# Kernel tuning notes

Measured on AMD Instinct MI355X. Metric: run time of the kernel, lower is better.

Reference implementation:

```python
import jax, jax.numpy as jnp
import numpy as np

VOCAB, D_MODEL, NHEAD, NLAYER, DIM_FF, MAX_LEN = 32000, 1024, 16, 6, 4096, 1024
B, L = 8, 1024
PAD_ID = 0
EPS = 1e-5


def _ln(x, g, b):
    m = x.mean(-1, keepdims=True)
    v = x.var(-1, keepdims=True)
    return (x - m) / jnp.sqrt(v + EPS) * g + b


def _mha(x, Wqkv, bqkv, Wo, bo, kpm):
    # x: [B,L,D]; Wqkv: [3D,D]; kpm: [B,L] bool (True = padded key)
    Bx, Lx, D = x.shape
    dh = D // NHEAD
    qkv = x @ Wqkv.T + bqkv                       # [B,L,3D]
    q, k, v = jnp.split(qkv, 3, axis=-1)
    sp = lambda t: t.reshape(Bx, Lx, NHEAD, dh).transpose(0, 2, 1, 3)  # [B,H,L,dh]
    q, k, v = sp(q), sp(k), sp(v)
    scores = jnp.einsum('bhqd,bhkd->bhqk', q, k) * (dh ** -0.5)
    scores = jnp.where(kpm[:, None, None, :], jnp.asarray(-1e9, scores.dtype), scores)
    attn = jax.nn.softmax(scores, axis=-1)        # explicit weights, as ForceWeightsMHA demands
    o = jnp.einsum('bhqk,bhkd->bhqd', attn, v)
    o = o.transpose(0, 2, 1, 3).reshape(Bx, Lx, D)
    return o @ Wo.T + bo


def setup_inputs() -> dict:
    key = jax.random.key(0)
    ks = jax.random.split(key, 20)
    s = 0.02
    n = lambda k, shp: (jax.random.normal(k, shp, dtype=jnp.float32) * s)
    inp = {
        'input_ids': jax.random.randint(ks[0], (B, L), 0, VOCAB, dtype=jnp.int64) if jax.config.jax_enable_x64 else jax.random.randint(ks[0], (B, L), 0, VOCAB).astype(jnp.int32),
        'tok_emb': n(ks[1], (VOCAB, D_MODEL)),
        'pos_emb': n(ks[2], (MAX_LEN, D_MODEL)),
        'Wqkv': n(ks[3], (NLAYER, 3 * D_MODEL, D_MODEL)),
        'bqkv': jnp.zeros((NLAYER, 3 * D_MODEL), jnp.float32),
        'Wo': n(ks[4], (NLAYER, D_MODEL, D_MODEL)),
        'bo': jnp.zeros((NLAYER, D_MODEL), jnp.float32),
        'ln1_g': jnp.ones((NLAYER, D_MODEL), jnp.float32),
        'ln1_b': jnp.zeros((NLAYER, D_MODEL), jnp.float32),
        'W1': n(ks[5], (NLAYER, DIM_FF, D_MODEL)),
        'b1': jnp.zeros((NLAYER, DIM_FF), jnp.float32),
        'W2': n(ks[6], (NLAYER, D_MODEL, DIM_FF)),
        'b2': jnp.zeros((NLAYER, D_MODEL), jnp.float32),
        'ln2_g': jnp.ones((NLAYER, D_MODEL), jnp.float32),
        'ln2_b': jnp.zeros((NLAYER, D_MODEL), jnp.float32),
        'head_ln_g': jnp.ones((D_MODEL,), jnp.float32),
        'head_ln_b': jnp.zeros((D_MODEL,), jnp.float32),
        'head_W': n(ks[7], (MAX_LEN, D_MODEL)),
        'head_b': jnp.zeros((MAX_LEN,), jnp.float32),
    }
    return inp


def reference(input_ids, tok_emb, pos_emb, Wqkv, bqkv, Wo, bo, ln1_g, ln1_b,
              W1, b1, W2, b2, ln2_g, ln2_b, head_ln_g, head_ln_b, head_W, head_b):
    Bx, Lx = input_ids.shape
    x = tok_emb[input_ids] + pos_emb[None, :Lx]           # [B,L,D]
    kpm = (input_ids == PAD_ID).at[:, 0].set(False)        # key padding mask, col 0 forced valid
    for i in range(NLAYER):                                # post-norm encoder layer (PyTorch default)
        x = _ln(x + _mha(x, Wqkv[i], bqkv[i], Wo[i], bo[i], kpm), ln1_g[i], ln1_b[i])
        ff = jax.nn.gelu(x @ W1[i].T + b1[i], approximate=False) @ W2[i].T + b2[i]
        x = _ln(x + ff, ln2_g[i], ln2_b[i])
    cls = x[:, 0, :]                                       # [B,D]
    return _ln(cls, head_ln_g, head_ln_b) @ head_W.T + head_b  # [B,MAX_LEN]
```

## Files before the change

### kernel.cpp

```cpp
#include <hip/hip_runtime.h>
#include <cstdint>

#define D_MODEL 1024
#define NHEAD   16
#define NLAYER  6
#define DIM_FF  4096
#define SEQ_B   8
#define SEQ_L   1024
#define TOKENS  (SEQ_B*SEQ_L)

typedef __bf16 v8bf  __attribute__((ext_vector_type(8)));
typedef __bf16 v4bf  __attribute__((ext_vector_type(4)));
typedef float  v4f   __attribute__((ext_vector_type(4)));

__device__ __forceinline__ void gl_lds16(const void* g, void* l) {
  __builtin_amdgcn_global_load_lds(
      (const __attribute__((address_space(1))) void*)g,
      (__attribute__((address_space(3))) void*)l, 16, 0, 0);
}

__global__ __launch_bounds__(256) void f2b_kernel(const float4* __restrict__ in,
                                                  ushort4* __restrict__ out, long n4) {
  long i = (long)blockIdx.x * 256 + threadIdx.x;
  long stride = (long)gridDim.x * 256;
  for (; i < n4; i += stride) {
    float4 v = in[i];
    v4bf r = { (__bf16)v.x, (__bf16)v.y, (__bf16)v.z, (__bf16)v.w };
    out[i] = *(ushort4*)&r;
  }
}

__global__ __launch_bounds__(256) void embed_kernel(const int* __restrict__ ids,
    const float4* __restrict__ tok, const float4* __restrict__ pos,
    float4* __restrict__ X, ushort4* __restrict__ Xb) {
  long i = (long)blockIdx.x * 256 + threadIdx.x;
  int d4 = (int)(i & 255);
  long bl = i >> 8;
  int l = (int)(bl & (SEQ_L - 1));
  int id = ids[bl];
  float4 t = tok[(long)id * 256 + d4];
  float4 p = pos[(long)l * 256 + d4];
  float4 v = {t.x + p.x, t.y + p.y, t.z + p.z, t.w + p.w};
  X[i] = v;
  v4bf r = { (__bf16)v.x, (__bf16)v.y, (__bf16)v.z, (__bf16)v.w };
  Xb[i] = *(ushort4*)&r;
}

__global__ __launch_bounds__(256) void maskb_kernel(const int* __restrict__ ids,
                                                    float* __restrict__ mb) {
  int i = blockIdx.x * 256 + threadIdx.x;
  mb[i] = (ids[i] == 0 && (i & 1023) != 0) ? -1e9f : 0.f;
}

template<int EPI>
__global__ __launch_bounds__(256) void gemm128(
    const unsigned short* __restrict__ A,
    const unsigned short* __restrict__ W,
    const float* __restrict__ bias,
    float* __restrict__ Cf, unsigned short* __restrict__ Cb,
    unsigned short* __restrict__ Vt,
    int M, int N, int K) {
  __shared__ unsigned short As[128 * 32];
  __shared__ unsigned short Bs[128 * 32];
  int tid = threadIdx.x;
  int wave = tid >> 6, lane = tid & 63;
  int l15 = lane & 15, quad = lane >> 4;

  int id = blockIdx.y * gridDim.x + blockIdx.x;
  int xcd = id & 7, sidx = id >> 3;
  int mt = xcd * 8 + (sidx & 7);
  int nt = sidx >> 3;
  int m0 = mt * 128, n0 = nt * 128;
  int wm = (wave >> 1) * 64, wn = (wave & 1) * 64;

  int srow = tid >> 2;
  int ssl  = (tid & 3) ^ ((srow >> 1) & 3);
  int sc8  = ssl << 3;
  const unsigned short* Ag0 = A + (long)(m0 + srow) * K + sc8;
  const unsigned short* Ag1 = A + (long)(m0 + srow + 64) * K + sc8;
  const unsigned short* Wg0 = W + (long)(n0 + srow) * K + sc8;
  const unsigned short* Wg1 = W + (long)(n0 + srow + 64) * K + sc8;
  unsigned short* As0 = As + tid * 8;
  unsigned short* As1 = As + tid * 8 + 2048;
  unsigned short* Bs0 = Bs + tid * 8;
  unsigned short* Bs1 = Bs + tid * 8 + 2048;

  const unsigned short* afp[4];
  const unsigned short* bfp[4];
  #pragma unroll
  for (int i = 0; i < 4; ++i) {
    int r = wm + i * 16 + l15;
    afp[i] = &As[r * 32 + ((quad ^ ((r >> 1) & 3)) << 3)];
    int rb = wn + i * 16 + l15;
    bfp[i] = &Bs[rb * 32 + ((quad ^ ((rb >> 1) & 3)) << 3)];
  }

  v4f acc[4][4];
  #pragma unroll
  for (int i = 0; i < 4; ++i)
    #pragma unroll
    for (int j = 0; j < 4; ++j) acc[i][j] = (v4f){0.f, 0.f, 0.f, 0.f};

  int ksteps = K >> 5;
  for (int ks = 0; ks < ksteps; ++ks) {
    int k0 = ks << 5;
    __syncthreads();
    gl_lds16(Ag0 + k0, As0);
    gl_lds16(Ag1 + k0, As1);
    gl_lds16(Wg0 + k0, Bs0);
    gl_lds16(Wg1 + k0, Bs1);
    __syncthreads();
    v8bf af[4], bf[4];
    #pragma unroll
    for (int i = 0; i < 4; ++i) af[i] = *(const v8bf*)afp[i];
    #pragma unroll
    for (int j = 0; j < 4; ++j) bf[j] = *(const v8bf*)bfp[j];
    #pragma unroll
    for (int i = 0; i < 4; ++i)
      #pragma unroll
      for (int j = 0; j < 4; ++j)
        acc[i][j] = __builtin_amdgcn_mfma_f32_16x16x32_bf16(af[i], bf[j], acc[i][j], 0, 0, 0);
  }

  #pragma unroll
  for (int i = 0; i < 4; ++i) {
    int crow0 = m0 + wm + i * 16 + quad * 4;
    #pragma unroll
    for (int j = 0; j < 4; ++j) {
      int col = n0 + wn + j * 16 + l15;
      float bv = bias[col];
      if (EPI == 3 && col >= 2048) {
        int hc = (col - 2048) >> 6, d = (col - 2048) & 63;
        int bb = crow0 >> 10, l = crow0 & 1023;
        v4bf pk = { (__bf16)(acc[i][j][0] + bv), (__bf16)(acc[i][j][1] + bv),
                    (__bf16)(acc[i][j][2] + bv), (__bf16)(acc[i][j][3] + bv) };
        *(ushort4*)&Vt[((long)((bb * 16 + hc) * 64 + d)) * 1024 + l] = *(ushort4*)&pk;
      } else {
        #pragma unroll
        for (int r = 0; r < 4; ++r) {
          float v = acc[i][j][r] + bv;
          if (EPI == 1) v = 0.5f * v * (1.f + erff(v * 0.70710678118f));
          long idx = (long)(crow0 + r) * N + col;
          if (EPI == 0) Cf[idx] = v;
          else          ((__bf16*)Cb)[idx] = (__bf16)v;
        }
      }
    }
  }
}

#define MM16(AF, BF, FO) \
  { _Pragma("unroll") for (int f_ = 0; f_ < 4; ++f_) { \
      _Pragma("unroll") for (int j_ = 0; j_ < 4; ++j_) \
        acc[(FO)+f_][j_] = __builtin_amdgcn_mfma_f32_16x16x32_bf16(AF[f_], BF[j_], acc[(FO)+f_][j_], 0, 0, 0); } }

#define STA(c,h,kt) { const unsigned short* s_ = pA + (long)(m0 + (h)*128)*K + ((long)(kt)<<6); \
  gl_lds16(s_,                 dAs + (c)*16384 + (h)*8192); \
  gl_lds16(s_ + ((long)K<<6),  dAs + (c)*16384 + (h)*8192 + 4096); }
#define STB(c,h,kt) { const unsigned short* s_ = pW + (long)(n0 + (h)*128)*K + ((long)(kt)<<6); \
  gl_lds16(s_,                 dBs + (c)*16384 + (h)*8192); \
  gl_lds16(s_ + ((long)K<<6),  dBs + (c)*16384 + (h)*8192 + 4096); }

#define LGKM0  asm volatile("s_waitcnt lgkmcnt(0)" ::: "memory")
#define VMCNT4 asm volatile("s_waitcnt vmcnt(4)" ::: "memory")
#define BARR   __builtin_amdgcn_s_barrier()
#define SCHED0 __builtin_amdgcn_sched_barrier(0)

template<int EPI>
__global__ __launch_bounds__(512, 2) void gemm256(
    const unsigned short* __restrict__ A,
    const unsigned short* __restrict__ W,
    const float* __restrict__ bias,
    unsigned short* __restrict__ Cb,
    unsigned short* __restrict__ Vt,
    int M, int N, int K) {
  __shared__ unsigned short As[2][16384];
  __shared__ unsigned short Bs[2][16384];
  int tid = threadIdx.x;
  int wave = tid >> 6, lane = tid & 63;
  int l15 = lane & 15, quad = lane >> 4;
  int wm = wave >> 2;
  int wn = wave & 3;

  int id = blockIdx.y * gridDim.x + blockIdx.x;
  int xcd = id & 7, sidx = id >> 3;
  int mt = xcd * 4 + (sidx & 3);
  int nt = sidx >> 2;
  int m0 = mt * 256, n0 = nt * 256;

  int srow = tid >> 3;
  int scol = ((tid & 7) ^ ((tid >> 4) & 7)) << 3;
  const unsigned short* pA = A + (long)srow * K + scol;
  const unsigned short* pW = W + (long)srow * K + scol;
  unsigned short* dAs = &As[0][0] + (tid << 3);
  unsigned short* dBs = &Bs[0][0] + (tid << 3);

  int offA[8], offB[4];
  #pragma unroll
  for (int f = 0; f < 8; ++f) {
    int r = wm * 128 + f * 16 + l15;
    offA[f] = r * 64 + ((quad ^ ((r >> 1) & 7)) << 3);
  }
  #pragma unroll
  for (int j = 0; j < 4; ++j) {
    int r = wn * 64 + j * 16 + l15;
    offB[j] = r * 64 + ((quad ^ ((r >> 1) & 7)) << 3);
  }

  v4f acc[8][4];
  #pragma unroll
  for (int f = 0; f < 8; ++f)
    #pragma unroll
    for (int j = 0; j < 4; ++j) acc[f][j] = (v4f){0.f, 0.f, 0.f, 0.f};

  int KT = K >> 6;
  STA(0, 0, 0); STA(0, 1, 0); STB(0, 0, 0); STB(0, 1, 0);
  STA(1, 0, 1); STA(1, 1, 1);
  VMCNT4; BARR; SCHED0;

  const unsigned short* as0 = &As[0][0];
  const unsigned short* bs0 = &Bs[0][0];
  const unsigned short* as1 = &As[1][0];
  const unsigned short* bs1 = &Bs[1][0];

  for (int tb = 0; tb < KT; tb += 2) {
    int kt2 = (tb + 2 < KT) ? tb + 2 : KT - 1;
    int kt3 = (tb + 3 < KT) ? tb + 3 : KT - 1;
    v8bf aA[4], aB[4], aC[4], aD[4], bA[4], bB[4];
    #pragma unroll
    for (int f = 0; f < 4; ++f) aA[f] = *(const v8bf*)(as0 + offA[f]);
    #pragma unroll
    for (int j = 0; j < 4; ++j) bA[j] = *(const v8bf*)(bs0 + offB[j]);
    #pragma unroll
    for (int j = 0; j < 4; ++j) bB[j] = *(const v8bf*)(bs0 + (offB[j] ^ 32));
    STB(1, 0, tb + 1);
    __builtin_amdgcn_s_setprio(1); MM16(aA, bA, 0); __builtin_amdgcn_s_setprio(0);
    #pragma unroll
    for (int f = 0; f < 4; ++f) aB[f] = *(const v8bf*)(as0 + (offA[f] ^ 32));
    STB(1, 1, tb + 1);
    __builtin_amdgcn_s_setprio(1); MM16(aB, bB, 0); __builtin_amdgcn_s_setprio(0);
    LGKM0; BARR; SCHED0;
    #pragma unroll
    for (int f = 0; f < 4; ++f) aC[f] = *(const v8bf*)(as0 + offA[4 + f]);
    #pragma unroll
    for (int f = 0; f < 4; ++f) aD[f] = *(const v8bf*)(as0 + (offA[4 + f] ^ 32));
    STB(0, 0, kt2);
    __builtin_amdgcn_s_setprio(1); MM16(aC, bA, 4); __builtin_amdgcn_s_setprio(0);
    STB(0, 1, kt2);
    __builtin_amdgcn_s_setprio(1); MM16(aD, bB, 4); __builtin_amdgcn_s_setprio(0);
    LGKM0; VMCNT4; BARR; SCHED0;
    #pragma unroll
    for (int f = 0; f < 4; ++f) aA[f] = *(const v8bf*)(as1 + offA[f]);
    #pragma unroll
    for (int j = 0; j < 4; ++j) bA[j] = *(const v8bf*)(bs1 + offB[j]);
    #pragma unroll
    for (int j = 0; j < 4; ++j) bB[j] = *(const v8bf*)(bs1 + (offB[j] ^ 32));
    STA(0, 0, kt2);
    __builtin_amdgcn_s_setprio(1); MM16(aA, bA, 0); __builtin_amdgcn_s_setprio(0);
    #pragma unroll
    for (int f = 0; f < 4; ++f) aB[f] = *(const v8bf*)(as1 + (offA[f] ^ 32));
    #pragma unroll
    for (int f = 0; f < 4; ++f) aC[f] = *(const v8bf*)(as1 + offA[4 + f]);
    #pragma unroll
    for (int f = 0; f < 4; ++f) aD[f] = *(const v8bf*)(as1 + (offA[4 + f] ^ 32));
    STA(0, 1, kt2);
    __builtin_amdgcn_s_setprio(1); MM16(aB, bB, 0); __builtin_amdgcn_s_setprio(0);
    LGKM0; BARR; SCHED0;
    STA(1, 0, kt3);
    __builtin_amdgcn_s_setprio(1); MM16(aC, bA, 4); __builtin_amdgcn_s_setprio(0);
    STA(1, 1, kt3);
    __builtin_amdgcn_s_setprio(1); MM16(aD, bB, 4); __builtin_amdgcn_s_setprio(0);
    VMCNT4; BARR; SCHED0;
  }

  #pragma unroll
  for (int f = 0; f < 8; ++f) {
    int crow0 = m0 + wm * 128 + f * 16 + quad * 4;
    #pragma unroll
    for (int j = 0; j < 4; ++j) {
      int col = n0 + wn * 64 + j * 16 + l15;
      float bv = bias[col];
      if (EPI == 3 && col >= 2048) {
        int hc = (col - 2048) >> 6, d = (col - 2048) & 63;
        int bb = crow0 >> 10, l = crow0 & 1023;
        v4bf pk = { (__bf16)(acc[f][j][0] + bv), (__bf16)(acc[f][j][1] + bv),
                    (__bf16)(acc[f][j][2] + bv), (__bf16)(acc[f][j][3] + bv) };
        *(ushort4*)&Vt[((long)((bb * 16 + hc) * 64 + d)) * 1024 + l] = *(ushort4*)&pk;
      } else {
        #pragma unroll
        for (int r = 0; r < 4; ++r) {
          float v = acc[f][j][r] + bv;
          if (EPI == 1) v = 0.5f * v * (1.f + erff(v * 0.70710678118f));
          ((__bf16*)Cb)[(long)(crow0 + r) * N + col] = (__bf16)v;
        }
      }
    }
  }
}

#define PSP 72
__global__ __launch_bounds__(256) void attn2(
    const unsigned short* __restrict__ QKVb,
    const unsigned short* __restrict__ Vtg,
    const float* __restrict__ mb,
    unsigned short* __restrict__ Ob) {
  __shared__ unsigned short Ks[64 * 64];
  __shared__ unsigned short Vs[64 * 64];
  __shared__ unsigned short Ps[4][16 * PSP];
  int tid = threadIdx.x, wave = tid >> 6, lane = tid & 63;
  int l15 = lane & 15, quad = lane >> 4;
  int b = blockIdx.z, h = blockIdx.y, q0 = blockIdx.x * 64;

  int qrow = q0 + wave * 16 + l15;
  const unsigned short* qb = QKVb + (long)(b * 1024 + qrow) * 3072 + h * 64;
  v8bf gq0 = *(const v8bf*)(qb + quad * 8);
  v8bf gq1 = *(const v8bf*)(qb + 32 + quad * 8);

  v8bf bones;
  #pragma unroll
  for (int j = 0; j < 8; ++j) bones[j] = (l15 == 0) ? (__bf16)1.0f : (__bf16)0.0f;

  float m_run[4], l_run[4];
  v4f O[4];
  #pragma unroll
  for (int r = 0; r < 4; ++r) { m_run[r] = -1e30f; l_run[r] = 0.f; }
  #pragma unroll
  for (int j = 0; j < 4; ++j) O[j] = (v4f){0.f, 0.f, 0.f, 0.f};

  const unsigned short* kgb = QKVb + (long)b * 1024 * 3072 + 1024 + h * 64;
  const unsigned short* vgb = Vtg + (long)((b * 16 + h) * 64) * 1024;
  const float* mrow = mb + b * 1024;

  int srow = tid >> 3;
  int ssl  = (tid & 7) ^ (srow & 7);
  int ph0 = (quad ^ (l15 & 7)) << 3;
  int ph1 = ((quad + 4) ^ (l15 & 7)) << 3;
  const float SC = 0.18033688011112042f;

  for (int k0 = 0; k0 < SEQ_L; k0 += 64) {
    __syncthreads();
    gl_lds16(kgb + (long)(k0 + srow) * 3072 + ssl * 8, &Ks[tid * 8]);
    gl_lds16(kgb + (long)(k0 + srow + 32) * 3072 + ssl * 8, &Ks[tid * 8 + 2048]);
    gl_lds16(vgb + (long)srow * 1024 + k0 + ssl * 8, &Vs[tid * 8]);
    gl_lds16(vgb + (long)(srow + 32) * 1024 + k0 + ssl * 8, &Vs[tid * 8 + 2048]);
    __syncthreads();

    float p[4][4], mr[4];
    #pragma unroll
    for (int r = 0; r < 4; ++r) mr[r] = -1e30f;
    #pragma unroll
    for (int t = 0; t < 4; ++t) {
      int kr = t * 16 + l15;
      v8bf kf0 = *(const v8bf*)&Ks[kr * 64 + ph0];
      v8bf kf1 = *(const v8bf*)&Ks[kr * 64 + ph1];
      v4f s = (v4f){0.f, 0.f, 0.f, 0.f};
      s = __builtin_amdgcn_mfma_f32_16x16x32_bf16(gq0, kf0, s, 0, 0, 0);
      s = __builtin_amdgcn_mfma_f32_16x16x32_bf16(gq1, kf1, s, 0, 0, 0);
      float bv = mrow[k0 + kr];
      #pragma unroll
      for (int r = 0; r < 4; ++r) {
        float sv = fmaf(s[r], SC, bv);
        p[t][r] = sv;
        mr[r] = fmaxf(mr[r], sv);
      }
    }
    #pragma unroll
    for (int r = 0; r < 4; ++r) {
      mr[r] = fmaxf(mr[r], __shfl_xor(mr[r], 1, 64));
      mr[r] = fmaxf(mr[r], __shfl_xor(mr[r], 2, 64));
      mr[r] = fmaxf(mr[r], __shfl_xor(mr[r], 4, 64));
      mr[r] = fmaxf(mr[r], __shfl_xor(mr[r], 8, 64));
    }
    float alpha[4];
    #pragma unroll
    for (int r = 0; r < 4; ++r) {
      float mn = fmaxf(m_run[r], mr[r]);
      alpha[r] = __builtin_amdgcn_exp2f(m_run[r] - mn);
      m_run[r] = mn;
    }
    #pragma unroll
    for (int t = 0; t < 4; ++t)
      #pragma unroll
      for (int r = 0; r < 4; ++r)
        p[t][r] = __builtin_amdgcn_exp2f(p[t][r] - m_run[r]);

    #pragma unroll
    for (int t = 0; t < 4; ++t)
      #pragma unroll
      for (int r = 0; r < 4; ++r)
        ((__bf16*)Ps[wave])[(quad * 4 + r) * PSP + t * 16 + l15] = (__bf16)p[t][r];
    v8bf pa0 = *(const v8bf*)&Ps[wave][l15 * PSP + quad * 8];
    v8bf pa1 = *(const v8bf*)&Ps[wave][l15 * PSP + 32 + quad * 8];

    v4f ss = (v4f){0.f, 0.f, 0.f, 0.f};
    ss = __builtin_amdgcn_mfma_f32_16x16x32_bf16(pa0, bones, ss, 0, 0, 0);
    ss = __builtin_amdgcn_mfma_f32_16x16x32_bf16(pa1, bones, ss, 0, 0, 0);

    #pragma unroll
    for (int j = 0; j < 4; ++j)
      #pragma unroll
      for (int r = 0; r < 4; ++r) O[j][r] *= alpha[r];
    #pragma unroll
    for (int j = 0; j < 4; ++j) {
      v8bf vf0 = *(const v8bf*)&Vs[(j * 16 + l15) * 64 + ph0];
      v8bf vf1 = *(const v8bf*)&Vs[(j * 16 + l15) * 64 + ph1];
      O[j] = __builtin_amdgcn_mfma_f32_16x16x32_bf16(pa0, vf0, O[j], 0, 0, 0);
      O[j] = __builtin_amdgcn_mfma_f32_16x16x32_bf16(pa1, vf1, O[j], 0, 0, 0);
    }
    #pragma unroll
    for (int r = 0; r < 4; ++r)
      l_run[r] = l_run[r] * alpha[r] + __shfl(ss[r], quad << 4, 64);
  }

  int qd = q0 + wave * 16 + quad * 4;
  #pragma unroll
  for (int r = 0; r < 4; ++r) {
    float inv = 1.f / l_run[r];
    #pragma unroll
    for (int j = 0; j < 4; ++j)
      ((__bf16*)Ob)[(long)(b * 1024 + qd + r) * 1024 + h * 64 + j * 16 + l15] =
          (__bf16)(O[j][r] * inv);
  }
}

__global__ __launch_bounds__(256) void add_ln(
    const float* __restrict__ Xin, const float* __restrict__ Yin,
    const float* __restrict__ g, const float* __restrict__ bta,
    float* __restrict__ outF, unsigned short* __restrict__ outB,
    long in_stride, long out_stride) {
  int row = blockIdx.x;
  const float* x = Xin + (long)row * in_stride;
  const float* y = Yin ? Yin + (long)row * 1024 : nullptr;
  int tid = threadIdx.x;
  float v[4];
  float s = 0.f, s2 = 0.f;
  #pragma unroll
  for (int j = 0; j < 4; ++j) {
    int d = j * 256 + tid;
    float t = x[d] + (y ? y[d] : 0.f);
    v[j] = t; s += t; s2 += t * t;
  }
  __shared__ float red[8];
  int lane = tid & 63, wave = tid >> 6;
  #pragma unroll
  for (int o = 32; o > 0; o >>= 1) { s += __shfl_down(s, o, 64); s2 += __shfl_down(s2, o, 64); }
  if (lane == 0) { red[wave] = s; red[4 + wave] = s2; }
  __syncthreads();
  s  = red[0] + red[1] + red[2] + red[3];
  s2 = red[4] + red[5] + red[6] + red[7];
  float mean = s * (1.f / 1024.f);
  float var  = s2 * (1.f / 1024.f) - mean * mean;
  float rstd = rsqrtf(var + 1e-5f);
  float* of = outF + (long)row * out_stride;
  unsigned short* ob = outB ? outB + (long)row * out_stride : nullptr;
  #pragma unroll
  for (int j = 0; j < 4; ++j) {
    int d = j * 256 + tid;
    float o = (v[j] - mean) * rstd * g[d] + bta[d];
    of[d] = o;
    if (ob) ((__bf16*)ob)[d] = (__bf16)o;
  }
}

__global__ __launch_bounds__(256) void head_kernel(
    const float* __restrict__ cls, const float* __restrict__ hW,
    const float* __restrict__ hb, float* __restrict__ out) {
  int n = blockIdx.x * 256 + threadIdx.x;
  int b = blockIdx.y;
  const float4* c4 = (const float4*)(cls + b * 1024);
  const float4* w4 = (const float4*)(hW + (long)n * 1024);
  float s = 0.f;
  #pragma unroll 8
  for (int d = 0; d < 256; ++d) {
    float4 a = c4[d], w = w4[d];
    s += a.x * w.x + a.y * w.y + a.z * w.z + a.w * w.w;
  }
  out[b * 1024 + n] = s + hb[n];
}

extern "C" void kernel_launch(void* const* d_in, const int* in_sizes, int n_in,
                              void* d_out, int out_size, void* d_ws, size_t ws_size,
                              hipStream_t stream) {
  const int*   ids  = (const int*)d_in[0];
  const float* tok  = (const float*)d_in[1];
  const float* pos  = (const float*)d_in[2];
  const float* Wqkv = (const float*)d_in[3];
  const float* bqkv = (const float*)d_in[4];
  const float* Wo   = (const float*)d_in[5];
  const float* bo   = (const float*)d_in[6];
  const float* ln1g = (const float*)d_in[7];
  const float* ln1b = (const float*)d_in[8];
  const float* W1   = (const float*)d_in[9];
  const float* b1   = (const float*)d_in[10];
  const float* W2   = (const float*)d_in[11];
  const float* b2   = (const float*)d_in[12];
  const float* ln2g = (const float*)d_in[13];
  const float* ln2b = (const float*)d_in[14];
  const float* hlng = (const float*)d_in[15];
  const float* hlnb = (const float*)d_in[16];
  const float* hW   = (const float*)d_in[17];
  const float* hb   = (const float*)d_in[18];
  float* out = (float*)d_out;

  char* ws = (char*)d_ws;
  size_t off = 0;
  auto alloc = [&](size_t bytes) {
    char* p = ws + off;
    off = (off + bytes + 255) & ~(size_t)255;
    return p;
  };
  unsigned short* Wqkv_b = (unsigned short*)alloc((size_t)NLAYER*3072*1024*2);
  unsigned short* Wo_b   = (unsigned short*)alloc((size_t)NLAYER*1024*1024*2);
  unsigned short* W1_b   = (unsigned short*)alloc((size_t)NLAYER*4096*1024*2);
  unsigned short* W2_b   = (unsigned short*)alloc((size_t)NLAYER*1024*4096*2);
  float*          X      = (float*)alloc((size_t)TOKENS*1024*4);
  unsigned short* Xb     = (unsigned short*)alloc((size_t)TOKENS*1024*2);
  unsigned short* Qb     = (unsigned short*)alloc((size_t)TOKENS*3072*2);
  unsigned short* Vtg    = (unsigned short*)alloc((size_t)TOKENS*1024*2);
  float*          Y      = (float*)alloc((size_t)TOKENS*1024*4);
  unsigned short* Ab     = (unsigned short*)alloc((size_t)TOKENS*1024*2);
  unsigned short* Gb     = Qb;
  float*          cls    = (float*)alloc(8*1024*4);
  float*          mb     = (float*)alloc(TOKENS*4);

  f2b_kernel<<<2048, 256, 0, stream>>>((const float4*)Wqkv, (ushort4*)Wqkv_b, (long)NLAYER*3072*1024/4);
  f2b_kernel<<<2048, 256, 0, stream>>>((const float4*)Wo,   (ushort4*)Wo_b,   (long)NLAYER*1024*1024/4);
  f2b_kernel<<<2048, 256, 0, stream>>>((const float4*)W1,   (ushort4*)W1_b,   (long)NLAYER*4096*1024/4);
  f2b_kernel<<<2048, 256, 0, stream>>>((const float4*)W2,   (ushort4*)W2_b,   (long)NLAYER*1024*4096/4);
  embed_kernel<<<(TOKENS*256)/256, 256, 0, stream>>>(ids, (const float4*)tok, (const float4*)pos,
                                                     (float4*)X, (ushort4*)Xb);
  maskb_kernel<<<TOKENS/256, 256, 0, stream>>>(ids, mb);

  for (int i = 0; i < NLAYER; ++i) {
    gemm256<3><<<dim3(3072/256, TOKENS/256), 512, 0, stream>>>(
        Xb, Wqkv_b + (size_t)i*3072*1024, bqkv + i*3072, Qb, Vtg, TOKENS, 3072, 1024);
    attn2<<<dim3(SEQ_L/64, NHEAD, SEQ_B), 256, 0, stream>>>(Qb, Vtg, mb, Ab);
    gemm128<0><<<dim3(1024/128, TOKENS/128), 256, 0, stream>>>(
        Ab, Wo_b + (size_t)i*1024*1024, bo + i*1024, Y, nullptr, nullptr, TOKENS, 1024, 1024);
    add_ln<<<TOKENS, 256, 0, stream>>>(X, Y, ln1g + i*1024, ln1b + i*1024, X, Xb, 1024L, 1024L);
    gemm256<1><<<dim3(4096/256, TOKENS/256), 512, 0, stream>>>(
        Xb, W1_b + (size_t)i*4096*1024, b1 + i*4096, Gb, nullptr, TOKENS, 4096, 1024);
    gemm128<0><<<dim3(1024/128, TOKENS/128), 256, 0, stream>>>(
        Gb, W2_b + (size_t)i*1024*4096, b2 + i*1024, Y, nullptr, nullptr, TOKENS, 1024, 4096);
    add_ln<<<TOKENS, 256, 0, stream>>>(X, Y, ln2g + i*1024, ln2b + i*1024, X, Xb, 1024L, 1024L);
  }
  add_ln<<<8, 256, 0, stream>>>(X, nullptr, hlng, hlnb, cls, nullptr, (long)SEQ_L*1024, 1024L);
  head_kernel<<<dim3(4, 8), 256, 0, stream>>>(cls, hW, hb, out);
}
```

Before: 3.203 ms.

## Replace N=1024 GEMMs with double-buffered 256x128 pipelined MFMA kernel

Adds gemm256n, a 512-thread kernel with 256x128 output tiles, 64-wide K steps, a double-buffered LDS pipeline using async global-to-LDS loads, and interleaved MFMA with setprio. It replaces the simple single-buffered gemm128 for the attention output projection and the FFN down projection, which write fp32 output. The aim is to hide memory latency and raise MFMA utilisation on the N=1024 GEMMs. The grid is halved (256 blocks), which could leave CUs underused, and the fused 32 KB A plus 16 KB B double buffer limits occupancy.

```diff
diff --git a/kernel.cpp b/kernel.cpp
--- a/kernel.cpp
+++ b/kernel.cpp
@@ -52,106 +52,13 @@
   mb[i] = (ids[i] == 0 && (i & 1023) != 0) ? -1e9f : 0.f;
 }
 
-template<int EPI>
-__global__ __launch_bounds__(256) void gemm128(
-    const unsigned short* __restrict__ A,
-    const unsigned short* __restrict__ W,
-    const float* __restrict__ bias,
-    float* __restrict__ Cf, unsigned short* __restrict__ Cb,
-    unsigned short* __restrict__ Vt,
-    int M, int N, int K) {
-  __shared__ unsigned short As[128 * 32];
-  __shared__ unsigned short Bs[128 * 32];
-  int tid = threadIdx.x;
-  int wave = tid >> 6, lane = tid & 63;
-  int l15 = lane & 15, quad = lane >> 4;
-
-  int id = blockIdx.y * gridDim.x + blockIdx.x;
-  int xcd = id & 7, sidx = id >> 3;
-  int mt = xcd * 8 + (sidx & 7);
-  int nt = sidx >> 3;
-  int m0 = mt * 128, n0 = nt * 128;
-  int wm = (wave >> 1) * 64, wn = (wave & 1) * 64;
-
-  int srow = tid >> 2;
-  int ssl  = (tid & 3) ^ ((srow >> 1) & 3);
-  int sc8  = ssl << 3;
-  const unsigned short* Ag0 = A + (long)(m0 + srow) * K + sc8;
-  const unsigned short* Ag1 = A + (long)(m0 + srow + 64) * K + sc8;
-  const unsigned short* Wg0 = W + (long)(n0 + srow) * K + sc8;
-  const unsigned short* Wg1 = W + (long)(n0 + srow + 64) * K + sc8;
-  unsigned short* As0 = As + tid * 8;
-  unsigned short* As1 = As + tid * 8 + 2048;
-  unsigned short* Bs0 = Bs + tid * 8;
-  unsigned short* Bs1 = Bs + tid * 8 + 2048;
-
-  const unsigned short* afp[4];
-  const unsigned short* bfp[4];
-  #pragma unroll
-  for (int i = 0; i < 4; ++i) {
-    int r = wm + i * 16 + l15;
-    afp[i] = &As[r * 32 + ((quad ^ ((r >> 1) & 3)) << 3)];
-    int rb = wn + i * 16 + l15;
-    bfp[i] = &Bs[rb * 32 + ((quad ^ ((rb >> 1) & 3)) << 3)];
-  }
-
-  v4f acc[4][4];
-  #pragma unroll
-  for (int i = 0; i < 4; ++i)
-    #pragma unroll
-    for (int j = 0; j < 4; ++j) acc[i][j] = (v4f){0.f, 0.f, 0.f, 0.f};
-
-  int ksteps = K >> 5;
-  for (int ks = 0; ks < ksteps; ++ks) {
-    int k0 = ks << 5;
-    __syncthreads();
-    gl_lds16(Ag0 + k0, As0);
-    gl_lds16(Ag1 + k0, As1);
-    gl_lds16(Wg0 + k0, Bs0);
-    gl_lds16(Wg1 + k0, Bs1);
-    __syncthreads();
-    v8bf af[4], bf[4];
-    #pragma unroll
-    for (int i = 0; i < 4; ++i) af[i] = *(const v8bf*)afp[i];
-    #pragma unroll
-    for (int j = 0; j < 4; ++j) bf[j] = *(const v8bf*)bfp[j];
-    #pragma unroll
-    for (int i = 0; i < 4; ++i)
-      #pragma unroll
-      for (int j = 0; j < 4; ++j)
-        acc[i][j] = __builtin_amdgcn_mfma_f32_16x16x32_bf16(af[i], bf[j], acc[i][j], 0, 0, 0);
-  }
-
-  #pragma unroll
-  for (int i = 0; i < 4; ++i) {
-    int crow0 = m0 + wm + i * 16 + quad * 4;
-    #pragma unroll
-    for (int j = 0; j < 4; ++j) {
-      int col = n0 + wn + j * 16 + l15;
-      float bv = bias[col];
-      if (EPI == 3 && col >= 2048) {
-        int hc = (col - 2048) >> 6, d = (col - 2048) & 63;
-        int bb = crow0 >> 10, l = crow0 & 1023;
-        v4bf pk = { (__bf16)(acc[i][j][0] + bv), (__bf16)(acc[i][j][1] + bv),
-                    (__bf16)(acc[i][j][2] + bv), (__bf16)(acc[i][j][3] + bv) };
-        *(ushort4*)&Vt[((long)((bb * 16 + hc) * 64 + d)) * 1024 + l] = *(ushort4*)&pk;
-      } else {
-        #pragma unroll
-        for (int r = 0; r < 4; ++r) {
-          float v = acc[i][j][r] + bv;
-          if (EPI == 1) v = 0.5f * v * (1.f + erff(v * 0.70710678118f));
-          long idx = (long)(crow0 + r) * N + col;
-          if (EPI == 0) Cf[idx] = v;
-          else          ((__bf16*)Cb)[idx] = (__bf16)v;
-        }
-      }
-    }
-  }
-}
-
 #define MM16(AF, BF, FO) \
   { _Pragma("unroll") for (int f_ = 0; f_ < 4; ++f_) { \
       _Pragma("unroll") for (int j_ = 0; j_ < 4; ++j_) \
+        acc[(FO)+f_][j_] = __builtin_amdgcn_mfma_f32_16x16x32_bf16(AF[f_], BF[j_], acc[(FO)+f_][j_], 0, 0, 0); } }
+#define MM8(AF, BF, FO) \
+  { _Pragma("unroll") for (int f_ = 0; f_ < 4; ++f_) { \
+      _Pragma("unroll") for (int j_ = 0; j_ < 2; ++j_) \
         acc[(FO)+f_][j_] = __builtin_amdgcn_mfma_f32_16x16x32_bf16(AF[f_], BF[j_], acc[(FO)+f_][j_], 0, 0, 0); } }
 
 #define STA(c,h,kt) { const unsigned short* s_ = pA + (long)(m0 + (h)*128)*K + ((long)(kt)<<6); \
@@ -160,6 +67,9 @@
 #define STB(c,h,kt) { const unsigned short* s_ = pW + (long)(n0 + (h)*128)*K + ((long)(kt)<<6); \
   gl_lds16(s_,                 dBs + (c)*16384 + (h)*8192); \
   gl_lds16(s_ + ((long)K<<6),  dBs + (c)*16384 + (h)*8192 + 4096); }
+#define STB2(c,kt) { const unsigned short* s_ = pW + (long)n0*K + ((long)(kt)<<6); \
+  gl_lds16(s_,                 dBs + (c)*8192); \
+  gl_lds16(s_ + ((long)K<<6),  dBs + (c)*8192 + 4096); }
 
 #define LGKM0  asm volatile("s_waitcnt lgkmcnt(0)" ::: "memory")
 #define VMCNT4 asm volatile("s_waitcnt vmcnt(4)" ::: "memory")
@@ -294,6 +204,123 @@
           ((__bf16*)Cb)[(long)(crow0 + r) * N + col] = (__bf16)v;
         }
       }
+    }
+  }
+}
+
+__global__ __launch_bounds__(512, 2) void gemm256n(
+    const unsigned short* __restrict__ A,
+    const unsigned short* __restrict__ W,
+    const float* __restrict__ bias,
+    float* __restrict__ Cf,
+    int M, int N, int K) {
+  __shared__ unsigned short As[2][16384];
+  __shared__ unsigned short Bs[2][8192];
+  int tid = threadIdx.x;
+  int wave = tid >> 6, lane = tid & 63;
+  int l15 = lane & 15, quad = lane >> 4;
+  int wm = wave >> 2;
+  int wn = wave & 3;
+
+  int id = blockIdx.y * gridDim.x + blockIdx.x;
+  int xcd = id & 7, sidx = id >> 3;
+  int mt = xcd * 4 + (sidx & 3);
+  int nt = sidx >> 2;
+  int m0 = mt * 256, n0 = nt * 128;
+
+  int srow = tid >> 3;
+  int scol = ((tid & 7) ^ ((tid >> 4) & 7)) << 3;
+  const unsigned short* pA = A + (long)srow * K + scol;
+  const unsigned short* pW = W + (long)srow * K + scol;
+  unsigned short* dAs = &As[0][0] + (tid << 3);
+  unsigned short* dBs = &Bs[0][0] + (tid << 3);
+
+  int offA[8], offB[2];
+  #pragma unroll
+  for (int f = 0; f < 8; ++f) {
+    int r = wm * 128 + f * 16 + l15;
+    offA[f] = r * 64 + ((quad ^ ((r >> 1) & 7)) << 3);
+  }
+  #pragma unroll
+  for (int j = 0; j < 2; ++j) {
+    int r = wn * 32 + j * 16 + l15;
+    offB[j] = r * 64 + ((quad ^ ((r >> 1) & 7)) << 3);
+  }
+
+  v4f acc[8][2];
+  #pragma unroll
+  for (int f = 0; f < 8; ++f)
+    #pragma unroll
+    for (int j = 0; j < 2; ++j) acc[f][j] = (v4f){0.f, 0.f, 0.f, 0.f};
+
+  int KT = K >> 6;
+  STA(0, 0, 0); STA(0, 1, 0); STB2(0, 0);
+  STA(1, 0, 1); STA(1, 1, 1);
+  VMCNT4; BARR; SCHED0;
+
+  const unsigned short* as0 = &As[0][0];
+  const unsigned short* bs0 = &Bs[0][0];
+  const unsigned short* as1 = &As[1][0];
+  const unsigned short* bs1 = &Bs[1][0];
+
+  for (int tb = 0; tb < KT; tb += 2) {
+    int kt2 = (tb + 2 < KT) ? tb + 2 : KT - 1;
+    int kt3 = (tb + 3 < KT) ? tb + 3 : KT - 1;
+    v8bf aA[4], aB[4], aC[4], aD[4], bA[2], bB[2];
+    #pragma unroll
+    for (int f = 0; f < 4; ++f) aA[f] = *(const v8bf*)(as0 + offA[f]);
+    #pragma unroll
+    for (int j = 0; j < 2; ++j) bA[j] = *(const v8bf*)(bs0 + offB[j]);
+    #pragma unroll
+    for (int j = 0; j < 2; ++j) bB[j] = *(const v8bf*)(bs0 + (offB[j] ^ 32));
+    STB2(1, tb + 1);
+    __builtin_amdgcn_s_setprio(1); MM8(aA, bA, 0); __builtin_amdgcn_s_setprio(0);
+    #pragma unroll
+    for (int f = 0; f < 4; ++f) aB[f] = *(const v8bf*)(as0 + (offA[f] ^ 32));
+    #pragma unroll
+    for (int f = 0; f < 4; ++f) aC[f] = *(const v8bf*)(as0 + offA[4 + f]);
+    #pragma unroll
+    for (int f = 0; f < 4; ++f) aD[f] = *(const v8bf*)(as0 + (offA[4 + f] ^ 32));
+    __builtin_amdgcn_s_setprio(1); MM8(aB, bB, 0); __builtin_amdgcn_s_setprio(0);
+    LGKM0; BARR; SCHED0;
+    STA(0, 0, kt2);
+    __builtin_amdgcn_s_setprio(1); MM8(aC, bA, 4); __builtin_amdgcn_s_setprio(0);
+    STA(0, 1, kt2);
+    __builtin_amdgcn_s_setprio(1); MM8(aD, bB, 4); __builtin_amdgcn_s_setprio(0);
+    VMCNT4; BARR; SCHED0;
+    #pragma unroll
+    for (int f = 0; f < 4; ++f) aA[f] = *(const v8bf*)(as1 + offA[f]);
+    #pragma unroll
+    for (int j = 0; j < 2; ++j) bA[j] = *(const v8bf*)(bs1 + offB[j]);
+    #pragma unroll
+    for (int j = 0; j < 2; ++j) bB[j] = *(const v8bf*)(bs1 + (offB[j] ^ 32));
+    STB2(0, kt2);
+    __builtin_amdgcn_s_setprio(1); MM8(aA, bA, 0); __builtin_amdgcn_s_setprio(0);
+    #pragma unroll
+    for (int f = 0; f < 4; ++f) aB[f] = *(const v8bf*)(as1 + (offA[f] ^ 32));
+    #pragma unroll
+    for (int f = 0; f < 4; ++f) aC[f] = *(const v8bf*)(as1 + offA[4 + f]);
+    #pragma unroll
+    for (int f = 0; f < 4; ++f) aD[f] = *(const v8bf*)(as1 + (offA[4 + f] ^ 32));
+    __builtin_amdgcn_s_setprio(1); MM8(aB, bB, 0); __builtin_amdgcn_s_setprio(0);
+    LGKM0; BARR; SCHED0;
+    STA(1, 0, kt3);
+    __builtin_amdgcn_s_setprio(1); MM8(aC, bA, 4); __builtin_amdgcn_s_setprio(0);
+    STA(1, 1, kt3);
+    __builtin_amdgcn_s_setprio(1); MM8(aD, bB, 4); __builtin_amdgcn_s_setprio(0);
+    VMCNT4; BARR; SCHED0;
+  }
+
+  #pragma unroll
+  for (int f = 0; f < 8; ++f) {
+    int crow0 = m0 + wm * 128 + f * 16 + quad * 4;
+    #pragma unroll
+    for (int j = 0; j < 2; ++j) {
+      int col = n0 + wn * 32 + j * 16 + l15;
+      float bv = bias[col];
+      #pragma unroll
+      for (int r = 0; r < 4; ++r)
+        Cf[(long)(crow0 + r) * N + col] = acc[f][j][r] + bv;
     }
   }
 }
@@ -535,13 +562,13 @@
     gemm256<3><<<dim3(3072/256, TOKENS/256), 512, 0, stream>>>(
         Xb, Wqkv_b + (size_t)i*3072*1024, bqkv + i*3072, Qb, Vtg, TOKENS, 3072, 1024);
     attn2<<<dim3(SEQ_L/64, NHEAD, SEQ_B), 256, 0, stream>>>(Qb, Vtg, mb, Ab);
-    gemm128<0><<<dim3(1024/128, TOKENS/128), 256, 0, stream>>>(
-        Ab, Wo_b + (size_t)i*1024*1024, bo + i*1024, Y, nullptr, nullptr, TOKENS, 1024, 1024);
+    gemm256n<<<dim3(1024/128, TOKENS/256), 512, 0, stream>>>(
+        Ab, Wo_b + (size_t)i*1024*1024, bo + i*1024, Y, TOKENS, 1024, 1024);
     add_ln<<<TOKENS, 256, 0, stream>>>(X, Y, ln1g + i*1024, ln1b + i*1024, X, Xb, 1024L, 1024L);
     gemm256<1><<<dim3(4096/256, TOKENS/256), 512, 0, stream>>>(
         Xb, W1_b + (size_t)i*4096*1024, b1 + i*4096, Gb, nullptr, TOKENS, 4096, 1024);
-    gemm128<0><<<dim3(1024/128, TOKENS/128), 256, 0, stream>>>(
-        Gb, W2_b + (size_t)i*1024*4096, b2 + i*1024, Y, nullptr, nullptr, TOKENS, 1024, 4096);
+    gemm256n<<<dim3(1024/128, TOKENS/256), 512, 0, stream>>>(
+        Gb, W2_b + (size_t)i*1024*4096, b2 + i*1024, Y, TOKENS, 1024, 4096);
     add_ln<<<TOKENS, 256, 0, stream>>>(X, Y, ln2g + i*1024, ln2b + i*1024, X, Xb, 1024L, 1024L);
   }
   add_ln<<<8, 256, 0, stream>>>(X, nullptr, hlng, hlnb, cls, nullptr, (long)SEQ_L*1024, 1024L);
```

Result: faster. 2.879 ms (-10.1%).
